# Optimization experiments

Hardware: AMD Instinct MI355X
Metric: run time of the kernel (lower is better)

The kernel has to match this reference:

```python
import jax, jax.numpy as jnp
import numpy as np

N_STEPS = 1000
LR_INNER = 0.1
LOG_CLAMP = -100.0  # torch BCE clamps log terms at -100


def _mlp(params, x):
    h = jax.nn.sigmoid(x @ params['w1'].T + params['b1'])   # [4,16]
    return jax.nn.sigmoid(h @ params['w2'].T + params['b2'])  # [4,1]


def _bce(y_pred, y_true):
    lp = jnp.clip(jnp.log(y_pred), LOG_CLAMP)
    lq = jnp.clip(jnp.log(1.0 - y_pred), LOG_CLAMP)
    return -jnp.mean(y_true * lp + (1.0 - y_true) * lq)


def setup_inputs() -> dict:
    key = jax.random.key(0)
    k1, k2 = jax.random.split(key)
    x = jnp.array([[0.0, 0.0], [0.0, 1.0], [1.0, 0.0], [1.0, 1.0]], dtype=jnp.float32)
    y_true = jnp.array([[0.0], [1.0], [1.0], [0.0]], dtype=jnp.float32)
    return {
        'x': x,
        'y_true': y_true,
        'w1': jax.random.normal(k1, (16, 2), dtype=jnp.float32),
        'b1': jnp.zeros((16,), dtype=jnp.float32),
        'w2': jax.random.normal(k2, (1, 16), dtype=jnp.float32),
        'b2': jnp.zeros((1,), dtype=jnp.float32),
    }


def reference(x, y_true, w1, b1, w2, b2):
    params = {'w1': w1, 'b1': b1, 'w2': w2, 'b2': b2}

    def loss_fn(p):
        return _bce(_mlp(p, x), y_true)

    def step(p, _):
        loss, grads = jax.value_and_grad(loss_fn)(p)
        p_new = jax.tree_util.tree_map(lambda a, g: a - LR_INNER * g, p, grads)  # sgd
        return p_new, loss

    params, losses = jax.lax.scan(step, params, None, length=N_STEPS)
    final_output = _mlp(params, x)  # [4,1]
    return final_output, losses
```

## Files before the change

### kernel.cpp

```cpp
#include <hip/hip_runtime.h>
#include <hip/hip_bf16.h>

#define N_STEPS 1000

#define DOT_STAGE(x, N) do { float _o;                                         \
    asm("s_nop 1\n\t"                                                          \
        "v_add_f32_dpp %0, %1, %1 row_ror:" #N " row_mask:0xf bank_mask:0xf"   \
        : "=v"(_o) : "v"(x));                                                  \
    x = _o; } while (0)

#define BWD_XLANE(d, dh, u, u1, u2, u3) \
    asm("s_nop 1\n\t"                                                                  \
        "v_add_f32_dpp %[d_], %[d_], %[d_] quad_perm:[1,0,3,2] row_mask:0xf bank_mask:0xf\n\t" \
        "v_mov_b32_dpp %[u1_], %[u_] quad_perm:[1,2,3,0] row_mask:0xf bank_mask:0xf\n\t"       \
        "v_add_f32_dpp %[h_], %[h_], %[h_] quad_perm:[1,0,3,2] row_mask:0xf bank_mask:0xf\n\t" \
        "v_mov_b32_dpp %[u2_], %[u_] quad_perm:[2,3,0,1] row_mask:0xf bank_mask:0xf\n\t"       \
        "v_mov_b32_dpp %[u3_], %[u_] quad_perm:[3,0,1,2] row_mask:0xf bank_mask:0xf\n\t"       \
        "v_add_f32_dpp %[d_], %[d_], %[d_] quad_perm:[2,3,0,1] row_mask:0xf bank_mask:0xf\n\t" \
        "v_add_f32_dpp %[h_], %[h_], %[h_] quad_perm:[2,3,0,1] row_mask:0xf bank_mask:0xf"     \
        : [d_] "+v"(d), [h_] "+v"(dh),                                                 \
          [u1_] "=&v"(u1), [u2_] "=&v"(u2), [u3_] "=&v"(u3)                            \
        : [u_] "v"(u))

#if defined(__has_builtin)
#  if __has_builtin(__builtin_amdgcn_permlane32_swap) && __has_builtin(__builtin_amdgcn_permlane16_swap)
#    define HAVE_PL 1
#  endif
#endif
#ifndef HAVE_PL
#  define HAVE_PL 0
#endif

template<bool PL> static __device__ __forceinline__ float redswap16(float x) {
    if (PL) {
#if HAVE_PL
        auto r = __builtin_amdgcn_permlane16_swap(__float_as_uint(x), __float_as_uint(x), false, false);
        return __uint_as_float(r[0]) + __uint_as_float(r[1]);
#endif
    }
    return x + __shfl_xor(x, 16);
}
template<bool PL> static __device__ __forceinline__ float redswap32(float x) {
    if (PL) {
#if HAVE_PL
        auto r = __builtin_amdgcn_permlane32_swap(__float_as_uint(x), __float_as_uint(x), false, false);
        return __uint_as_float(r[0]) + __uint_as_float(r[1]);
#endif
    }
    return x + __shfl_xor(x, 32);
}

#define NEG_LOG2E (-1.4426950408889634f)
#define LRS       (0.14426950408889634f)

template<bool PL>
static __device__ __forceinline__ void run_all(
    int tid, float Xr0, float Xr1, float cr,
    float M0, float M1, float M2, float M3,
    float Y0, float Y1, float Y2, float Y3,
    float z1s, float w2s, float B,
    float* __restrict__ p_lds, float* __restrict__ out)
{
    const float lrs_seed = (tid < 4) ? LRS : 0.0f;

    #pragma unroll 2
    for (int s = 0; s < N_STEPS; ++s) {
        float e1 = __builtin_amdgcn_exp2f(z1s);
        float h  = __builtin_amdgcn_rcpf(1.0f + e1);
        float vp = (w2s * h) * (1.0f - h);

        float t = fmaf(h, w2s, B);
        DOT_STAGE(t, 4);
        DOT_STAGE(t, 8);
        t = redswap16<PL>(t);
        t = redswap32<PL>(t);
        float e2 = __builtin_amdgcn_exp2f(t);
        float p  = __builtin_amdgcn_rcpf(1.0f + e2);

        p_lds[4 * s + (tid & 3)] = p;

        float d  = fmaf(0.25f, p, cr);
        float u  = d * vp;
        float dh = d * h;
        float u1, u2, u3;
        BWD_XLANE(d, dh, u, u1, u2, u3);

        z1s = fmaf(M0, u,  z1s);
        z1s = fmaf(M1, u1, z1s);
        z1s = fmaf(M2, u2, z1s);
        z1s = fmaf(M3, u3, z1s);
        w2s = fmaf(LRS,      dh, w2s);
        B   = fmaf(lrs_seed, d,  B);
    }

    {
        float e1 = __builtin_amdgcn_exp2f(z1s);
        float h  = __builtin_amdgcn_rcpf(1.0f + e1);
        float t  = fmaf(h, w2s, B);
        DOT_STAGE(t, 4);
        DOT_STAGE(t, 8);
        t = redswap16<PL>(t);
        t = redswap32<PL>(t);
        float p = __builtin_amdgcn_rcpf(1.0f + __builtin_amdgcn_exp2f(t));
        if (tid < 4) out[tid] = p;
    }

    __syncthreads();

    for (int s2 = tid; s2 < N_STEPS; s2 += 64) {
        const float4 pv = *(const float4*)&p_lds[s2 * 4];
        float pp[4] = {pv.x, pv.y, pv.z, pv.w};
        float yy[4] = {Y0, Y1, Y2, Y3};
        float sum = 0.0f;
        #pragma unroll
        for (int i = 0; i < 4; ++i) {
            float pi = pp[i];
            float qi = 1.0f - pi;
            float lp = fmaxf(__logf(pi), -100.0f);
            float lq = fmaxf(__logf(qi), -100.0f);
            sum += yy[i] * lp + (1.0f - yy[i]) * lq;
        }
        out[4 + s2] = -(sum * 0.25f);
    }
}

__global__ __launch_bounds__(64, 1) void xor_train_v9(
    const void* __restrict__ x_p,
    const void* __restrict__ y_p,
    const void* __restrict__ w1_p,
    const void* __restrict__ s16a_p,
    const void* __restrict__ s16b_p,
    const void* __restrict__ b2_p,
    float* __restrict__ out)
{
    __shared__ float p_lds[N_STEPS * 4];

    const int tid = threadIdx.x;
    const int r   = tid & 3;
    const int j   = tid >> 2;

    const bool in_bf16 = (((const float*)y_p)[1] != 1.0f);
    const bool a_is_b1 = (((const unsigned*)s16a_p)[0] == 0u);
    const void* b1_p = a_is_b1 ? s16a_p : s16b_p;
    const void* w2_p = a_is_b1 ? s16b_p : s16a_p;

    float X[4][2], Y[4];
    float w10, w11, b1v, w2v, b2v;
    if (in_bf16) {
        const __hip_bfloat16* xb = (const __hip_bfloat16*)x_p;
        const __hip_bfloat16* yb = (const __hip_bfloat16*)y_p;
        #pragma unroll
        for (int i = 0; i < 4; ++i) {
            X[i][0] = __bfloat162float(xb[2 * i + 0]);
            X[i][1] = __bfloat162float(xb[2 * i + 1]);
            Y[i]    = __bfloat162float(yb[i]);
        }
        const __hip_bfloat16* w1b = (const __hip_bfloat16*)w1_p;
        w10 = __bfloat162float(w1b[2 * j + 0]);
        w11 = __bfloat162float(w1b[2 * j + 1]);
        b1v = __bfloat162float(((const __hip_bfloat16*)b1_p)[j]);
        w2v = __bfloat162float(((const __hip_bfloat16*)w2_p)[j]);
        b2v = __bfloat162float(((const __hip_bfloat16*)b2_p)[0]);
    } else {
        const float* xf = (const float*)x_p;
        const float* yf = (const float*)y_p;
        #pragma unroll
        for (int i = 0; i < 4; ++i) {
            X[i][0] = xf[2 * i + 0];
            X[i][1] = xf[2 * i + 1];
            Y[i]    = yf[i];
        }
        w10 = ((const float*)w1_p)[2 * j + 0];
        w11 = ((const float*)w1_p)[2 * j + 1];
        b1v = ((const float*)b1_p)[j];
        w2v = ((const float*)w2_p)[j];
        b2v = ((const float*)b2_p)[0];
    }

    const float Xr0 = X[r][0], Xr1 = X[r][1];
    const float cr  = -0.25f * Y[r];

    const int r1 = (r + 1) & 3, r2 = (r + 2) & 3, r3 = (r + 3) & 3;
    #define SELX(idx, c) ((idx) == 0 ? X[0][c] : (idx) == 1 ? X[1][c] : (idx) == 2 ? X[2][c] : X[3][c])
    const float M0 = -0.1f * (1.0f + Xr0 * Xr0 + Xr1 * Xr1);
    const float M1 = -0.1f * (1.0f + Xr0 * SELX(r1, 0) + Xr1 * SELX(r1, 1));
    const float M2 = -0.1f * (1.0f + Xr0 * SELX(r2, 0) + Xr1 * SELX(r2, 1));
    const float M3 = -0.1f * (1.0f + Xr0 * SELX(r3, 0) + Xr1 * SELX(r3, 1));
    #undef SELX

    const float z1u = fmaf(Xr1, w11, fmaf(Xr0, w10, b1v));
    const float z1s = NEG_LOG2E * z1u;
    const float w2s = NEG_LOG2E * w2v;
    const float B   = (tid < 4) ? (NEG_LOG2E * b2v) : 0.0f;

    bool pl_ok = false;
#if HAVE_PL
    {
        float tv = (float)(1 << (tid >> 4));
        float fs = redswap32<true>(redswap16<true>(tv));
        pl_ok = (bool)__all(fs == 15.0f);
    }
#endif

    if (pl_ok)
        run_all<true>(tid, Xr0, Xr1, cr, M0, M1, M2, M3,
                      Y[0], Y[1], Y[2], Y[3], z1s, w2s, B, p_lds, out);
    else
        run_all<false>(tid, Xr0, Xr1, cr, M0, M1, M2, M3,
                       Y[0], Y[1], Y[2], Y[3], z1s, w2s, B, p_lds, out);
}

extern "C" void kernel_launch(void* const* d_in, const int* in_sizes, int n_in,
                              void* d_out, int out_size, void* d_ws, size_t ws_size,
                              hipStream_t stream) {
    const void* xv = nullptr; const void* yv = nullptr; const void* w1 = nullptr;
    const void* b2 = nullptr;
    const void* s16[2] = {nullptr, nullptr}; int n16 = 0;
    for (int i = 0; i < n_in; ++i) {
        switch (in_sizes[i]) {
            case 8:  xv = d_in[i]; break;
            case 4:  yv = d_in[i]; break;
            case 32: w1 = d_in[i]; break;
            case 1:  b2 = d_in[i]; break;
            case 16: if (n16 < 2) s16[n16++] = d_in[i]; break;
            default: break;
        }
    }
    if (!xv || !yv || !w1 || !b2 || n16 != 2) {
        xv = d_in[0]; yv = d_in[1]; w1 = d_in[2];
        s16[0] = d_in[3]; s16[1] = d_in[4]; b2 = d_in[5];
    }
    float* out = (float*)d_out;

    hipLaunchKernelGGL(xor_train_v9, dim3(1), dim3(64), 0, stream,
                       xv, yv, w1, s16[0], s16[1], b2, out);
}
```

Baseline: 111.6 us.

## Restructure first-layer update to shorten the per-step dependency chain

Splits the first-layer pre-activation update into a part that depends only on vp and labels, computed while the output reduction is in flight, and a part linear in p applied after the sigmoid. This takes the d*vp product and its cross-lane rotations off the serial critical path that follows the forward reduction. The cost is extra multiplies and DPP moves per step, plus a rearranged floating-point sum whose rounding can differ slightly from before.

Result: slower. 128.4 us (+15.0%).

```diff
diff --git a/kernel.cpp b/kernel.cpp
--- a/kernel.cpp
+++ b/kernel.cpp
@@ -9,18 +9,18 @@
         : "=v"(_o) : "v"(x));                                                  \
     x = _o; } while (0)
 
-#define BWD_XLANE(d, dh, u, u1, u2, u3) \
+#define QSUM2(d, dh) \
     asm("s_nop 1\n\t"                                                                  \
         "v_add_f32_dpp %[d_], %[d_], %[d_] quad_perm:[1,0,3,2] row_mask:0xf bank_mask:0xf\n\t" \
-        "v_mov_b32_dpp %[u1_], %[u_] quad_perm:[1,2,3,0] row_mask:0xf bank_mask:0xf\n\t"       \
         "v_add_f32_dpp %[h_], %[h_], %[h_] quad_perm:[1,0,3,2] row_mask:0xf bank_mask:0xf\n\t" \
-        "v_mov_b32_dpp %[u2_], %[u_] quad_perm:[2,3,0,1] row_mask:0xf bank_mask:0xf\n\t"       \
-        "v_mov_b32_dpp %[u3_], %[u_] quad_perm:[3,0,1,2] row_mask:0xf bank_mask:0xf\n\t"       \
+        "s_nop 1\n\t"                                                                  \
         "v_add_f32_dpp %[d_], %[d_], %[d_] quad_perm:[2,3,0,1] row_mask:0xf bank_mask:0xf\n\t" \
         "v_add_f32_dpp %[h_], %[h_], %[h_] quad_perm:[2,3,0,1] row_mask:0xf bank_mask:0xf"     \
-        : [d_] "+v"(d), [h_] "+v"(dh),                                                 \
-          [u1_] "=&v"(u1), [u2_] "=&v"(u2), [u3_] "=&v"(u3)                            \
-        : [u_] "v"(u))
+        : [d_] "+v"(d), [h_] "+v"(dh))
+
+#define QROT1(x) __uint_as_float((unsigned)__builtin_amdgcn_update_dpp(0, (int)__float_as_uint(x), 0x39, 0xf, 0xf, false))
+#define QROT2(x) __uint_as_float((unsigned)__builtin_amdgcn_update_dpp(0, (int)__float_as_uint(x), 0x4E, 0xf, 0xf, false))
+#define QROT3(x) __uint_as_float((unsigned)__builtin_amdgcn_update_dpp(0, (int)__float_as_uint(x), 0x93, 0xf, 0xf, false))
 
 #if defined(__has_builtin)
 #  if __has_builtin(__builtin_amdgcn_permlane32_swap) && __has_builtin(__builtin_amdgcn_permlane16_swap)
@@ -55,8 +55,9 @@
 
 template<bool PL>
 static __device__ __forceinline__ void run_all(
-    int tid, float Xr0, float Xr1, float cr,
-    float M0, float M1, float M2, float M3,
+    int tid, float cr,
+    float Q0, float Q1, float Q2, float Q3,
+    float crq0, float crq1, float crq2, float crq3,
     float Y0, float Y1, float Y2, float Y3,
     float z1s, float w2s, float B,
     float* __restrict__ p_lds, float* __restrict__ out)
@@ -74,21 +75,32 @@
         DOT_STAGE(t, 8);
         t = redswap16<PL>(t);
         t = redswap32<PL>(t);
+
+        float vp1 = QROT1(vp), vp2 = QROT2(vp), vp3 = QROT3(vp);
+        float A0 = Q0 * vp;
+        float A1 = Q1 * vp1;
+        float A2 = Q2 * vp2;
+        float A3 = Q3 * vp3;
+        float zb = fmaf(A0, crq0, z1s);
+        zb = fmaf(A1, crq1, zb);
+        zb = fmaf(A2, crq2, zb);
+        zb = fmaf(A3, crq3, zb);
+
         float e2 = __builtin_amdgcn_exp2f(t);
         float p  = __builtin_amdgcn_rcpf(1.0f + e2);
 
         p_lds[4 * s + (tid & 3)] = p;
 
         float d  = fmaf(0.25f, p, cr);
-        float u  = d * vp;
         float dh = d * h;
-        float u1, u2, u3;
-        BWD_XLANE(d, dh, u, u1, u2, u3);
-
-        z1s = fmaf(M0, u,  z1s);
-        z1s = fmaf(M1, u1, z1s);
-        z1s = fmaf(M2, u2, z1s);
-        z1s = fmaf(M3, u3, z1s);
+
+        float p1 = QROT1(p), p2 = QROT2(p), p3 = QROT3(p);
+        z1s = fmaf(A0, p,  zb);
+        z1s = fmaf(A1, p1, z1s);
+        z1s = fmaf(A2, p2, z1s);
+        z1s = fmaf(A3, p3, z1s);
+
+        QSUM2(d, dh);
         w2s = fmaf(LRS,      dh, w2s);
         B   = fmaf(lrs_seed, d,  B);
     }
@@ -124,7 +136,7 @@
     }
 }
 
-__global__ __launch_bounds__(64, 1) void xor_train_v9(
+__global__ __launch_bounds__(64, 1) void xor_train_v10(
     const void* __restrict__ x_p,
     const void* __restrict__ y_p,
     const void* __restrict__ w1_p,
@@ -182,11 +194,17 @@
 
     const int r1 = (r + 1) & 3, r2 = (r + 2) & 3, r3 = (r + 3) & 3;
     #define SELX(idx, c) ((idx) == 0 ? X[0][c] : (idx) == 1 ? X[1][c] : (idx) == 2 ? X[2][c] : X[3][c])
-    const float M0 = -0.1f * (1.0f + Xr0 * Xr0 + Xr1 * Xr1);
-    const float M1 = -0.1f * (1.0f + Xr0 * SELX(r1, 0) + Xr1 * SELX(r1, 1));
-    const float M2 = -0.1f * (1.0f + Xr0 * SELX(r2, 0) + Xr1 * SELX(r2, 1));
-    const float M3 = -0.1f * (1.0f + Xr0 * SELX(r3, 0) + Xr1 * SELX(r3, 1));
+    #define SELY(idx)    ((idx) == 0 ? Y[0]    : (idx) == 1 ? Y[1]    : (idx) == 2 ? Y[2]    : Y[3])
+    const float Q0 = -0.025f * (1.0f + Xr0 * Xr0 + Xr1 * Xr1);
+    const float Q1 = -0.025f * (1.0f + Xr0 * SELX(r1, 0) + Xr1 * SELX(r1, 1));
+    const float Q2 = -0.025f * (1.0f + Xr0 * SELX(r2, 0) + Xr1 * SELX(r2, 1));
+    const float Q3 = -0.025f * (1.0f + Xr0 * SELX(r3, 0) + Xr1 * SELX(r3, 1));
+    const float crq0 = -Y[r];
+    const float crq1 = -SELY(r1);
+    const float crq2 = -SELY(r2);
+    const float crq3 = -SELY(r3);
     #undef SELX
+    #undef SELY
 
     const float z1u = fmaf(Xr1, w11, fmaf(Xr0, w10, b1v));
     const float z1s = NEG_LOG2E * z1u;
@@ -203,10 +221,10 @@
 #endif
 
     if (pl_ok)
-        run_all<true>(tid, Xr0, Xr1, cr, M0, M1, M2, M3,
+        run_all<true>(tid, cr, Q0, Q1, Q2, Q3, crq0, crq1, crq2, crq3,
                       Y[0], Y[1], Y[2], Y[3], z1s, w2s, B, p_lds, out);
     else
-        run_all<false>(tid, Xr0, Xr1, cr, M0, M1, M2, M3,
+        run_all<false>(tid, cr, Q0, Q1, Q2, Q3, crq0, crq1, crq2, crq3,
                        Y[0], Y[1], Y[2], Y[3], z1s, w2s, B, p_lds, out);
 }
 
@@ -232,6 +250,6 @@
     }
     float* out = (float*)d_out;
 
-    hipLaunchKernelGGL(xor_train_v9, dim3(1), dim3(64), 0, stream,
+    hipLaunchKernelGGL(xor_train_v10, dim3(1), dim3(64), 0, stream,
                        xv, yv, w1, s16[0], s16[1], b2, out);
 }
```
